# Optimization experiments

Measured on AMD Instinct MI355X. Metric: run time of the kernel, lower is better.

## Reference

```python
import jax, jax.numpy as jnp
import numpy as np

N_ENT = 100000   # n_entities
N_REL = 40       # n_relations_ckg
D = 64           # embed_dim
L = 3            # n_layers
E = 1000000      # number of CKG triples (edges)


def setup_inputs() -> dict:
    key = jax.random.key(0)
    k = jax.random.split(key, 6)
    xavier = np.sqrt(6.0 / (D + D))  # xavier_uniform for square Linear
    return {
        "heads": jax.random.randint(k[0], (E,), 0, N_ENT),
        "rels": jax.random.randint(k[1], (E,), 0, N_REL),
        "tails": jax.random.randint(k[2], (E,), 0, N_ENT),
        "entity_embed": 0.01 * jax.random.normal(k[3], (N_ENT, D), dtype=jnp.float32),
        "rel_embeds": 0.01 * jax.random.normal(k[4], (L, N_REL, D), dtype=jnp.float32),
        "Ws": (jax.random.uniform(k[5], (L, D, D), minval=-1.0, maxval=1.0) * xavier).astype(jnp.float32),
    }


def _kgat_layer(h, heads, rels, tails, rel_emb, W):
    # h: [N, D]; heads/rels/tails: [E]; rel_emb: [n_rel, D]; W: [D, D] (nn.Linear weight)
    n = h.shape[0]
    e_h = h[heads]            # [E, D] gather
    e_t = h[tails]            # [E, D] gather
    e_r = rel_emb[rels]       # [E, D] gather
    # pi(h,r,t) = e_t . tanh(e_h + e_r)
    score = jnp.sum(e_t * jnp.tanh(e_h + e_r), axis=-1)          # [E]
    score = score - jax.lax.stop_gradient(jnp.max(score))        # global shift (detach)
    score_exp = jnp.exp(score)                                   # [E]
    score_sum = jax.ops.segment_sum(score_exp, heads, num_segments=n)  # [N]
    attn = score_exp / (score_sum[heads] + 1e-10)                # [E] per-head softmax
    agg = jax.ops.segment_sum(attn[:, None] * e_t, heads, num_segments=n)  # [N, D]
    out = (h + agg) @ W.T                                        # Linear, no bias
    return jax.nn.leaky_relu(out, negative_slope=0.2)            # dropout = identity (eval)


def reference(heads, rels, tails, entity_embed, rel_embeds, Ws):
    h = entity_embed
    all_layers = [h]
    for l in range(rel_embeds.shape[0]):
        h = _kgat_layer(h, heads, rels, tails, rel_embeds[l], Ws[l])
        all_layers.append(h)
    return jnp.concatenate(all_layers, axis=-1)  # [N, D*(L+1)]
```

## Files before the change

### kernel.cpp

```cpp
#include <hip/hip_runtime.h>

#define DD 64
#define ROW 256
#define CHUNK 1024

__global__ void k_copy_count(const float* __restrict__ ent, float* __restrict__ out,
                             const int* __restrict__ heads, int* __restrict__ counts,
                             int n_rows, int nE) {
    int idx = blockIdx.x * blockDim.x + threadIdx.x;
    int total = n_rows * 16;
    if (idx < total) {
        int n = idx >> 4, q = idx & 15;
        const float4* src = (const float4*)(ent + (long)n * DD);
        float4* dst = (float4*)(out + (long)n * ROW);
        dst[q] = src[q];
    }
    if (idx < nE) {
        atomicAdd(counts + heads[idx], 1);
    }
}

__global__ __launch_bounds__(256) void k_scan_chunk(
        const int* __restrict__ counts, int* __restrict__ offs,
        int* __restrict__ partials, int n) {
    __shared__ int lds[256];
    int base = blockIdx.x * CHUNK;
    int t = threadIdx.x;
    int c[4]; int sum = 0;
    #pragma unroll
    for (int j = 0; j < 4; ++j) {
        int i = base + t * 4 + j;
        c[j] = (i < n) ? counts[i] : 0;
        sum += c[j];
    }
    lds[t] = sum; __syncthreads();
    for (int d = 1; d < 256; d <<= 1) {
        int v = (t >= d) ? lds[t - d] : 0;
        __syncthreads();
        lds[t] += v;
        __syncthreads();
    }
    int excl = lds[t] - sum;
    if (t == 255) partials[blockIdx.x] = lds[255];
    int run = excl;
    #pragma unroll
    for (int j = 0; j < 4; ++j) {
        int i = base + t * 4 + j;
        if (i < n) offs[i] = run;
        run += c[j];
    }
}

__global__ __launch_bounds__(256) void k_scan_add(
        int* __restrict__ offs, int* __restrict__ running,
        const int* __restrict__ partials, int n, int nE, int nchunks) {
    __shared__ int lds[128];
    int t = threadIdx.x;
    if (t < 128) {
        int v = (t < nchunks) ? partials[t] : 0;
        lds[t] = v;
    }
    __syncthreads();
    for (int d = 1; d < 128; d <<= 1) {
        int u = (t < 128 && t >= d) ? lds[t - d] : 0;
        __syncthreads();
        if (t < 128) lds[t] += u;
        __syncthreads();
    }
    int i = blockIdx.x * 256 + t;
    if (i < n) {
        int ck = i >> 10;
        int excl = (ck == 0) ? 0 : lds[ck - 1];
        int v = offs[i] + excl;
        offs[i] = v;
        running[i] = v;
    } else if (i == n) {
        offs[n] = nE;
    }
}

__global__ void k_scatter(const int* __restrict__ heads, const int* __restrict__ rels,
                          const int* __restrict__ tails, int* __restrict__ running,
                          int* __restrict__ packed, int nE) {
    int e = blockIdx.x * 256 + threadIdx.x;
    if (e >= nE) return;
    int h = heads[e];
    int pos = atomicAdd(running + h, 1);
    packed[pos] = tails[e] | (rels[e] << 20);
}

__global__ __launch_bounds__(256) void k_layer(
        const int* __restrict__ offs, const int* __restrict__ packed,
        const float* __restrict__ hbase, const float* __restrict__ relemb,
        const float* __restrict__ W, float* __restrict__ outbase,
        int n_heads, int nE) {
    __shared__ float Wt[DD * 65];
    __shared__ float xs[4][DD];
    for (int idx = threadIdx.x; idx < DD * DD; idx += 256)
        Wt[(idx & 63) * 65 + (idx >> 6)] = W[idx];
    __syncthreads();

    int w = threadIdx.x >> 6, lane = threadIdx.x & 63;
    int g = lane >> 4, s = lane & 15;

    for (int hd = blockIdx.x * 4 + w; hd < n_heads; hd += gridDim.x * 4) {
        const float4 eh4 = *(const float4*)(hbase + (long)hd * ROW + 4 * s);
        float4 acc = make_float4(0.f, 0.f, 0.f, 0.f);
        float ssum = 0.f;
        int p0 = offs[hd], pe = offs[hd + 1];

        for (int cbase = p0; cbase < pe; cbase += 64) {
            int clen = min(pe - cbase, 64);
            int vAll = packed[min(cbase + lane, nE - 1)];

            int i0 = (g < clen) ? g : 0;
            int i1 = (4 + g < clen) ? 4 + g : 0;
            int v0 = __shfl(vAll, i0);
            int v1 = __shfl(vAll, i1);
            float4 tt0 = *(const float4*)(hbase + (long)(v0 & 0xFFFFF) * ROW + 4 * s);
            float4 rr0 = *(const float4*)(relemb + (v0 >> 20) * DD + 4 * s);
            float4 tt1 = *(const float4*)(hbase + (long)(v1 & 0xFFFFF) * ROW + 4 * s);
            float4 rr1 = *(const float4*)(relemb + (v1 >> 20) * DD + 4 * s);

            for (int i = 0; i < clen; i += 8) {
                int ia = i + 8 + g;  ia = (ia < clen) ? ia : 0;
                int ib = i + 12 + g; ib = (ib < clen) ? ib : 0;
                int va = __shfl(vAll, ia);
                int vb = __shfl(vAll, ib);
                float4 tta = *(const float4*)(hbase + (long)(va & 0xFFFFF) * ROW + 4 * s);
                float4 rra = *(const float4*)(relemb + (va >> 20) * DD + 4 * s);
                float4 ttb = *(const float4*)(hbase + (long)(vb & 0xFFFFF) * ROW + 4 * s);
                float4 rrb = *(const float4*)(relemb + (vb >> 20) * DD + 4 * s);

                {
                    float sc = 0.f;
                    #pragma unroll
                    for (int q = 0; q < 4; ++q) {
                        float xq = (&eh4.x)[q] + (&rr0.x)[q];
                        float t = __expf(2.f * xq);
                        float th = 1.f - 2.f * __builtin_amdgcn_rcpf(t + 1.f);
                        sc += (&tt0.x)[q] * th;
                    }
                    #pragma unroll
                    for (int off = 1; off <= 8; off <<= 1) sc += __shfl_xor(sc, off);
                    float se = ((i + g) < clen) ? __expf(sc) : 0.f;
                    ssum += se;
                    acc.x += se * tt0.x; acc.y += se * tt0.y;
                    acc.z += se * tt0.z; acc.w += se * tt0.w;
                }
                {
                    float sc = 0.f;
                    #pragma unroll
                    for (int q = 0; q < 4; ++q) {
                        float xq = (&eh4.x)[q] + (&rr1.x)[q];
                        float t = __expf(2.f * xq);
                        float th = 1.f - 2.f * __builtin_amdgcn_rcpf(t + 1.f);
                        sc += (&tt1.x)[q] * th;
                    }
                    #pragma unroll
                    for (int off = 1; off <= 8; off <<= 1) sc += __shfl_xor(sc, off);
                    float se = ((i + 4 + g) < clen) ? __expf(sc) : 0.f;
                    ssum += se;
                    acc.x += se * tt1.x; acc.y += se * tt1.y;
                    acc.z += se * tt1.z; acc.w += se * tt1.w;
                }
                tt0 = tta; rr0 = rra; tt1 = ttb; rr1 = rrb;
            }
        }

        #pragma unroll
        for (int off = 16; off <= 32; off <<= 1) {
            acc.x += __shfl_xor(acc.x, off);
            acc.y += __shfl_xor(acc.y, off);
            acc.z += __shfl_xor(acc.z, off);
            acc.w += __shfl_xor(acc.w, off);
            ssum  += __shfl_xor(ssum,  off);
        }
        float inv = 1.f / (ssum + 1e-10f);
        float4 x4;
        x4.x = eh4.x + acc.x * inv;  x4.y = eh4.y + acc.y * inv;
        x4.z = eh4.z + acc.z * inv;  x4.w = eh4.w + acc.w * inv;
        if (g == 0) *(float4*)(&xs[w][4 * s]) = x4;

        float y = 0.f;
        const float* xw = xs[w];
        #pragma unroll
        for (int k4 = 0; k4 < DD; k4 += 4) {
            float4 xv = *(const float4*)(xw + k4);
            y += xv.x * Wt[(k4 + 0) * 65 + lane];
            y += xv.y * Wt[(k4 + 1) * 65 + lane];
            y += xv.z * Wt[(k4 + 2) * 65 + lane];
            y += xv.w * Wt[(k4 + 3) * 65 + lane];
        }
        y = y >= 0.f ? y : 0.2f * y;
        outbase[(long)hd * ROW + lane] = y;
    }
}

extern "C" void kernel_launch(void* const* d_in, const int* in_sizes, int n_in,
                              void* d_out, int out_size, void* d_ws, size_t ws_size,
                              hipStream_t stream) {
    const int*   heads = (const int*)d_in[0];
    const int*   rels  = (const int*)d_in[1];
    const int*   tails = (const int*)d_in[2];
    const float* ent   = (const float*)d_in[3];
    const float* rel   = (const float*)d_in[4];
    const float* Ws    = (const float*)d_in[5];
    float* out = (float*)d_out;

    const int nE = in_sizes[0];
    const int N  = in_sizes[3] / DD;
    const int L  = in_sizes[5] / (DD * DD);
    const int NREL = in_sizes[4] / (L * DD);

    int* offs    = (int*)d_ws;
    int* running = offs + (N + 1);
    int* packed  = running + N;
    int* partials = packed + nE - 128;

    dim3 blk(256);
    int nchunks = (N + CHUNK - 1) / CHUNK;
    int fuse_total = max(N * 16, nE);

    hipMemsetAsync(running, 0, (size_t)N * sizeof(int), stream);
    k_copy_count<<<(fuse_total + 255) / 256, blk, 0, stream>>>(ent, out, heads, running, N, nE);
    k_scan_chunk<<<nchunks, blk, 0, stream>>>(running, offs, partials, N);
    k_scan_add<<<(N + 1 + 255) / 256, blk, 0, stream>>>(offs, running, partials, N, nE, nchunks);
    k_scatter<<<(nE + 255) / 256, blk, 0, stream>>>(heads, rels, tails, running, packed, nE);

    for (int l = 0; l < L; ++l) {
        k_layer<<<2048, blk, 0, stream>>>(
            offs, packed, out + l * DD, rel + (long)l * NREL * DD,
            Ws + (long)l * DD * DD, out + (l + 1) * DD, N, nE);
    }
}
```

Before: 478.4 us.

## Fuse CSR build stages into one cooperative kernel with grid syncs

```diff
diff --git a/kernel.cpp b/kernel.cpp
--- a/kernel.cpp
+++ b/kernel.cpp
@@ -1,92 +1,98 @@
 #include <hip/hip_runtime.h>
+#include <hip/hip_cooperative_groups.h>
+namespace cg = cooperative_groups;
 
 #define DD 64
 #define ROW 256
 #define CHUNK 1024
 
-__global__ void k_copy_count(const float* __restrict__ ent, float* __restrict__ out,
-                             const int* __restrict__ heads, int* __restrict__ counts,
-                             int n_rows, int nE) {
-    int idx = blockIdx.x * blockDim.x + threadIdx.x;
-    int total = n_rows * 16;
-    if (idx < total) {
-        int n = idx >> 4, q = idx & 15;
-        const float4* src = (const float4*)(ent + (long)n * DD);
-        float4* dst = (float4*)(out + (long)n * ROW);
-        dst[q] = src[q];
-    }
-    if (idx < nE) {
-        atomicAdd(counts + heads[idx], 1);
-    }
-}
-
-__global__ __launch_bounds__(256) void k_scan_chunk(
-        const int* __restrict__ counts, int* __restrict__ offs,
-        int* __restrict__ partials, int n) {
+__global__ __launch_bounds__(256) void k_csr_build(
+        const float* __restrict__ ent, float* __restrict__ out,
+        const int* __restrict__ heads, const int* __restrict__ rels,
+        const int* __restrict__ tails, int* __restrict__ offs,
+        int* __restrict__ running, int* __restrict__ packed,
+        int* __restrict__ partials, int n, int nE, int nchunks) {
+    cg::grid_group grid = cg::this_grid();
     __shared__ int lds[256];
-    int base = blockIdx.x * CHUNK;
     int t = threadIdx.x;
-    int c[4]; int sum = 0;
-    #pragma unroll
-    for (int j = 0; j < 4; ++j) {
-        int i = base + t * 4 + j;
-        c[j] = (i < n) ? counts[i] : 0;
-        sum += c[j];
-    }
-    lds[t] = sum; __syncthreads();
-    for (int d = 1; d < 256; d <<= 1) {
-        int v = (t >= d) ? lds[t - d] : 0;
+    long tid = (long)blockIdx.x * 256 + t;
+    long gsz = (long)gridDim.x * 256;
+
+    for (long i = tid; i < n; i += gsz) running[i] = 0;
+    for (long idx = tid; idx < (long)n * 16; idx += gsz) {
+        long r = idx >> 4; int q = (int)(idx & 15);
+        ((float4*)(out + r * ROW))[q] = ((const float4*)(ent + r * DD))[q];
+    }
+    __threadfence();
+    grid.sync();
+
+    for (long e = tid; e < nE; e += gsz)
+        atomicAdd(running + heads[e], 1);
+    __threadfence();
+    grid.sync();
+
+    for (int c = blockIdx.x; c < nchunks; c += gridDim.x) {
+        int base = c * CHUNK;
+        int cc[4]; int sum = 0;
+        #pragma unroll
+        for (int j = 0; j < 4; ++j) {
+            int i = base + t * 4 + j;
+            cc[j] = (i < n) ? running[i] : 0;
+            sum += cc[j];
+        }
+        lds[t] = sum; __syncthreads();
+        for (int d = 1; d < 256; d <<= 1) {
+            int v = (t >= d) ? lds[t - d] : 0;
+            __syncthreads();
+            lds[t] += v;
+            __syncthreads();
+        }
+        int excl = lds[t] - sum;
+        if (t == 255) partials[c] = lds[255];
+        int run = excl;
+        #pragma unroll
+        for (int j = 0; j < 4; ++j) {
+            int i = base + t * 4 + j;
+            if (i < n) offs[i] = run;
+            run += cc[j];
+        }
         __syncthreads();
-        lds[t] += v;
+    }
+    __threadfence();
+    grid.sync();
+
+    if (blockIdx.x == 0) {
+        int v = (t < 128 && t < nchunks) ? partials[t] : 0;
+        if (t < 128) lds[t] = v;
         __syncthreads();
-    }
-    int excl = lds[t] - sum;
-    if (t == 255) partials[blockIdx.x] = lds[255];
-    int run = excl;
-    #pragma unroll
-    for (int j = 0; j < 4; ++j) {
-        int i = base + t * 4 + j;
-        if (i < n) offs[i] = run;
-        run += c[j];
-    }
-}
-
-__global__ __launch_bounds__(256) void k_scan_add(
-        int* __restrict__ offs, int* __restrict__ running,
-        const int* __restrict__ partials, int n, int nE, int nchunks) {
-    __shared__ int lds[128];
-    int t = threadIdx.x;
-    if (t < 128) {
-        int v = (t < nchunks) ? partials[t] : 0;
-        lds[t] = v;
-    }
-    __syncthreads();
-    for (int d = 1; d < 128; d <<= 1) {
-        int u = (t < 128 && t >= d) ? lds[t - d] : 0;
-        __syncthreads();
-        if (t < 128) lds[t] += u;
-        __syncthreads();
-    }
-    int i = blockIdx.x * 256 + t;
-    if (i < n) {
-        int ck = i >> 10;
-        int excl = (ck == 0) ? 0 : lds[ck - 1];
-        int v = offs[i] + excl;
-        offs[i] = v;
-        running[i] = v;
-    } else if (i == n) {
-        offs[n] = nE;
-    }
-}
-
-__global__ void k_scatter(const int* __restrict__ heads, const int* __restrict__ rels,
-                          const int* __restrict__ tails, int* __restrict__ running,
-                          int* __restrict__ packed, int nE) {
-    int e = blockIdx.x * 256 + threadIdx.x;
-    if (e >= nE) return;
-    int h = heads[e];
-    int pos = atomicAdd(running + h, 1);
-    packed[pos] = tails[e] | (rels[e] << 20);
+        for (int d = 1; d < 128; d <<= 1) {
+            int u = (t < 128 && t >= d) ? lds[t - d] : 0;
+            __syncthreads();
+            if (t < 128) lds[t] += u;
+            __syncthreads();
+        }
+        if (t < 128) partials[t] = lds[t] - v;
+    }
+    __threadfence();
+    grid.sync();
+
+    for (long i = tid; i <= n; i += gsz) {
+        if (i < n) {
+            int v = offs[i] + partials[i >> 10];
+            offs[i] = v;
+            running[i] = v;
+        } else {
+            offs[n] = nE;
+        }
+    }
+    __threadfence();
+    grid.sync();
+
+    for (long e = tid; e < nE; e += gsz) {
+        int h = heads[e];
+        int pos = atomicAdd(running + h, 1);
+        packed[pos] = tails[e] | (rels[e] << 20);
+    }
 }
 
 __global__ __launch_bounds__(256) void k_layer(
@@ -200,12 +206,12 @@
 extern "C" void kernel_launch(void* const* d_in, const int* in_sizes, int n_in,
                               void* d_out, int out_size, void* d_ws, size_t ws_size,
                               hipStream_t stream) {
-    const int*   heads = (const int*)d_in[0];
-    const int*   rels  = (const int*)d_in[1];
-    const int*   tails = (const int*)d_in[2];
     const float* ent   = (const float*)d_in[3];
     const float* rel   = (const float*)d_in[4];
     const float* Ws    = (const float*)d_in[5];
+    const int* heads = (const int*)d_in[0];
+    const int* rels  = (const int*)d_in[1];
+    const int* tails = (const int*)d_in[2];
     float* out = (float*)d_out;
 
     const int nE = in_sizes[0];
@@ -218,18 +224,19 @@
     int* packed  = running + N;
     int* partials = packed + nE - 128;
 
-    dim3 blk(256);
     int nchunks = (N + CHUNK - 1) / CHUNK;
-    int fuse_total = max(N * 16, nE);
-
-    hipMemsetAsync(running, 0, (size_t)N * sizeof(int), stream);
-    k_copy_count<<<(fuse_total + 255) / 256, blk, 0, stream>>>(ent, out, heads, running, N, nE);
-    k_scan_chunk<<<nchunks, blk, 0, stream>>>(running, offs, partials, N);
-    k_scan_add<<<(N + 1 + 255) / 256, blk, 0, stream>>>(offs, running, partials, N, nE, nchunks);
-    k_scatter<<<(nE + 255) / 256, blk, 0, stream>>>(heads, rels, tails, running, packed, nE);
+
+    {
+        void* args[] = { (void*)&ent, (void*)&out, (void*)&heads, (void*)&rels,
+                         (void*)&tails, (void*)&offs, (void*)&running,
+                         (void*)&packed, (void*)&partials,
+                         (void*)&N, (void*)&nE, (void*)&nchunks };
+        hipLaunchCooperativeKernel((const void*)k_csr_build,
+                                   dim3(1024), dim3(256), args, 0, stream);
+    }
 
     for (int l = 0; l < L; ++l) {
-        k_layer<<<2048, blk, 0, stream>>>(
+        k_layer<<<2048, dim3(256), 0, stream>>>(
             offs, packed, out + l * DD, rel + (long)l * NREL * DD,
             Ws + (long)l * DD * DD, out + (l + 1) * DD, N, nE);
     }
```

Result: slower. 1.307 ms (+173.2%).
